# Kernel optimization log

Hardware: AMD Instinct MI355X
Metric: run time of the kernel (lower is better)

## Reference

```python
import jax, jax.numpy as jnp
import numpy as np

NUM_SYMBOLS = 100000
EMBED_DIM = 256
DIM = 2 * EMBED_DIM          # 512
NUM_HEADS = 4
HEAD_DIM = DIM // NUM_HEADS  # 128
N = 100                      # hard-coded neighbor count in source
EPS = 1e-5


def layernorm(x, g, b):
    mu = jnp.mean(x, axis=-1, keepdims=True)
    var = jnp.var(x, axis=-1, keepdims=True)
    return (x - mu) * jax.lax.rsqrt(var + EPS) * g + b


def setup_inputs() -> dict:
    key = jax.random.key(0)
    ks = jax.random.split(key, 12)
    B, FEW = 512, 2
    connections = jax.random.randint(ks[0], (B, FEW, N, 2), 0, NUM_SYMBOLS)
    mask = jax.random.randint(ks[1], (B * FEW, N, N), 0, 2).astype(jnp.int32)
    s = 0.02
    emb = jax.random.normal(ks[2], (NUM_SYMBOLS + 1, EMBED_DIM), jnp.float32) * s
    qkv_w = jax.random.normal(ks[3], (3 * DIM, DIM), jnp.float32) * s
    qkv_b = jnp.zeros((3 * DIM,), jnp.float32)
    proj_w = jax.random.normal(ks[4], (DIM, DIM), jnp.float32) * s
    proj_b = jnp.zeros((DIM,), jnp.float32)
    ln1_g = jnp.ones((DIM,), jnp.float32); ln1_b = jnp.zeros((DIM,), jnp.float32)
    ln2_g = jnp.ones((DIM,), jnp.float32); ln2_b = jnp.zeros((DIM,), jnp.float32)
    fc_w = jax.random.normal(ks[5], (DIM // 2, DIM), jnp.float32) * s
    fc_b = jnp.zeros((DIM // 2,), jnp.float32)
    return {"connections": connections, "mask": mask, "emb": emb,
            "qkv_w": qkv_w, "qkv_b": qkv_b, "proj_w": proj_w, "proj_b": proj_b,
            "ln1_g": ln1_g, "ln1_b": ln1_b, "ln2_g": ln2_g, "ln2_b": ln2_b,
            "fc_w": fc_w, "fc_b": fc_b}


def reference(connections, mask, emb, qkv_w, qkv_b, proj_w, proj_b,
              ln1_g, ln1_b, ln2_g, ln2_b, fc_w, fc_b):
    # embedding gathers for (relation, entity) pairs
    rel = emb[connections[..., 0]]          # [B, few, N, E]
    ent = emb[connections[..., 1]]          # [B, few, N, E]
    x = jnp.concatenate([rel, ent], axis=-1).reshape(-1, N, DIM)  # [BN, N, C]
    m = mask.reshape(-1, N, N)

    xn = layernorm(x, ln1_g, ln1_b)
    qkv = xn @ qkv_w.T + qkv_b              # [BN, N, 3C]
    BN = xn.shape[0]
    qkv = qkv.reshape(BN, N, 3, NUM_HEADS, HEAD_DIM).transpose(2, 0, 3, 1, 4)
    q, k, v = qkv[0], qkv[1], qkv[2]        # [BN, H, N, hd]

    scale = HEAD_DIM ** -0.5
    attn = jnp.einsum('bhnd,bhmd->bhnm', q, k) * scale
    attn = jnp.where(m[:, None] == 0, -1e9, attn)
    attn = jax.nn.softmax(attn, axis=-1)    # [BN, H, N, N]

    y = jnp.einsum('bhnm,bhmd->bhnd', attn, v)
    y = y.transpose(0, 2, 1, 3).reshape(BN, N, DIM)
    y = y @ proj_w.T + proj_b               # [BN, N, C]

    # attn.mean(dim=2): mean over query axis -> [BN, H, N]; bmm with y
    wc = jnp.einsum('bhn,bnc->bhc', attn.mean(axis=2), y)   # [BN, H, C]
    out = layernorm(wc, ln2_g, ln2_b) @ fc_w.T + fc_b       # [BN, H, C//2]
    return out
```

## Files before the change

kernel.cpp:

```cpp
#include <hip/hip_runtime.h>
#include <stdint.h>

typedef __attribute__((ext_vector_type(8))) short bf16x8;
typedef __attribute__((ext_vector_type(4))) float f32x4;
typedef __attribute__((ext_vector_type(4))) unsigned int u32x4;
typedef __attribute__((ext_vector_type(4))) unsigned short u16x4;

typedef const void __attribute__((address_space(1))) gvoid_t;
typedef void __attribute__((address_space(3))) lvoid_t;

__device__ __forceinline__ unsigned short f2bf(float f) {
  union { float f; unsigned int u; } v; v.f = f;
  unsigned int u = v.u;
  u += 0x7fffu + ((u >> 16) & 1u);
  return (unsigned short)(u >> 16);
}
__device__ __forceinline__ float bf2f(unsigned short h) {
  union { unsigned int u; float f; } v; v.u = ((unsigned int)h) << 16;
  return v.f;
}
__device__ __forceinline__ void load_lds16(const void* g, void* l) {
  __builtin_amdgcn_global_load_lds((gvoid_t*)g, (lvoid_t*)l, 16, 0, 0);
}

#define GATE6() asm volatile("s_waitcnt vmcnt(6)" ::: "memory")
#define GATE4() asm volatile("s_waitcnt vmcnt(4)" ::: "memory")
#define GATE0() asm volatile("s_waitcnt vmcnt(0)" ::: "memory")
#define BARRIER()                    \
  do {                               \
    asm volatile("" ::: "memory");   \
    __builtin_amdgcn_s_barrier();    \
    asm volatile("" ::: "memory");   \
  } while (0)

__global__ __launch_bounds__(256) void k_cvt(const float* __restrict__ src,
                                             unsigned short* __restrict__ dst, int n) {
  int i = blockIdx.x * 256 + threadIdx.x;
  if (i < n) dst[i] = f2bf(src[i]);
}

__global__ __launch_bounds__(256) void k_maskpack(const int* __restrict__ mask,
                                                  unsigned int* __restrict__ bm) {
  const int lane = threadIdx.x & 63;
  const int wv = (blockIdx.x << 2) + (threadIdx.x >> 6);
  const int r0 = wv * 16;
  for (int i = 0; i < 16; ++i) {
    const int r = r0 + i;
    const size_t base = (size_t)r * 100;
    const int c0 = mask[base + lane];
    int c1 = 0;
    if (lane < 36) c1 = mask[base + 64 + lane];
    const unsigned long long b0 = __ballot(c0 != 0);
    const unsigned long long b1 = __ballot(c1 != 0);
    if (lane == 0) {
      u32x4 v;
      v[0] = (unsigned int)b0; v[1] = (unsigned int)(b0 >> 32);
      v[2] = (unsigned int)b1; v[3] = (unsigned int)(b1 >> 32);
      *(u32x4*)(bm + (size_t)r * 4) = v;
    }
  }
}

__global__ __launch_bounds__(256) void k_gather_ln(const int* __restrict__ conn,
                                                   const float* __restrict__ emb,
                                                   const float* __restrict__ g1,
                                                   const float* __restrict__ b1,
                                                   unsigned short* __restrict__ xn,
                                                   int row0) {
  const int lane = threadIdx.x & 63;
  const int wid = threadIdx.x >> 6;
  const int rloc = blockIdx.x * 4 + wid;
  const int row = row0 + rloc;
  const int rel = conn[row * 2 + 0];
  const int ent = conn[row * 2 + 1];
  const float4 r4 = *(const float4*)(emb + (size_t)rel * 256 + lane * 4);
  const float4 e4 = *(const float4*)(emb + (size_t)ent * 256 + lane * 4);
  float rv[4] = {r4.x, r4.y, r4.z, r4.w};
  float ev[4] = {e4.x, e4.y, e4.z, e4.w};
  float s = 0.f, ss = 0.f;
#pragma unroll
  for (int j = 0; j < 4; ++j) { s += rv[j] + ev[j]; ss += rv[j] * rv[j] + ev[j] * ev[j]; }
#pragma unroll
  for (int d = 1; d < 64; d <<= 1) { s += __shfl_xor(s, d, 64); ss += __shfl_xor(ss, d, 64); }
  const float mu = s * (1.f / 512.f);
  const float var = ss * (1.f / 512.f) - mu * mu;
  const float rs = rsqrtf(var + 1e-5f);
  const float4 ga = *(const float4*)(g1 + lane * 4);
  const float4 gb = *(const float4*)(g1 + 256 + lane * 4);
  const float4 ba = *(const float4*)(b1 + lane * 4);
  const float4 bb = *(const float4*)(b1 + 256 + lane * 4);
  float gav[4] = {ga.x, ga.y, ga.z, ga.w}, gbv[4] = {gb.x, gb.y, gb.z, gb.w};
  float bav[4] = {ba.x, ba.y, ba.z, ba.w}, bbv[4] = {bb.x, bb.y, bb.z, bb.w};
  u16x4 o0, o1;
#pragma unroll
  for (int j = 0; j < 4; ++j) {
    o0[j] = f2bf((rv[j] - mu) * rs * gav[j] + bav[j]);
    o1[j] = f2bf((ev[j] - mu) * rs * gbv[j] + bbv[j]);
  }
  unsigned short* orow = xn + (size_t)rloc * 512;
  *(u16x4*)(orow + lane * 4) = o0;
  *(u16x4*)(orow + 256 + lane * 4) = o1;
}

__global__ __launch_bounds__(256, 2) void k_gemm4(const unsigned short* __restrict__ A,
                                                  const unsigned short* __restrict__ W,
                                                  const float* __restrict__ bias,
                                                  unsigned short* __restrict__ C,
                                                  int N, int K, int ntiles, int nwg) {
  __shared__ __align__(16) unsigned short ldsA[3][256 * 32];
  __shared__ __align__(16) unsigned short ldsB[3][128 * 32];

  const int orig = blockIdx.x;
  const int q = nwg >> 3, r = nwg & 7;
  const int xcd = orig & 7, idx = orig >> 3;
  const int wg = (xcd < r ? xcd * (q + 1) : r * (q + 1) + (xcd - r) * q) + idx;
  const int mtile = wg / ntiles, ntile = wg % ntiles;

  const int t = threadIdx.x, lane = t & 63, wid = t >> 6;
  const int wm = wid >> 1, wn = wid & 1;
  const size_t Abase = (size_t)mtile * 256 * K;
  const size_t Wbase = (size_t)ntile * 128 * K;
  const int NT = K >> 5;

  f32x4 acc[8][4];
#pragma unroll
  for (int i = 0; i < 8; ++i)
#pragma unroll
    for (int j = 0; j < 4; ++j) acc[i][j] = (f32x4){0.f, 0.f, 0.f, 0.f};

  const int sr0 = t >> 2;
  auto stage = [&](int buf, int kt) {
#pragma unroll
    for (int it = 0; it < 4; ++it) {
      const int row = it * 64 + sr0;
      const int cl = (t & 3) ^ ((row >> 1) & 3);
      load_lds16(A + Abase + (size_t)row * K + kt * 32 + cl * 8, &ldsA[buf][it * 2048 + t * 8]);
    }
#pragma unroll
    for (int it = 0; it < 2; ++it) {
      const int row = it * 64 + sr0;
      const int cl = (t & 3) ^ ((row >> 1) & 3);
      load_lds16(W + Wbase + (size_t)row * K + kt * 32 + cl * 8, &ldsB[buf][it * 2048 + t * 8]);
    }
  };

  stage(0, 0);
  stage(1, 1);

  int cur = 0;
  for (int kt = 0; kt < NT; ++kt) {
    if (kt + 1 < NT) { GATE6(); } else { GATE0(); }
    BARRIER();
    if (kt + 2 < NT) {
      int s2 = cur + 2; if (s2 >= 3) s2 -= 3;
      stage(s2, kt + 2);
    }
    bf16x8 af[8], bfr[4];
#pragma unroll
    for (int mi = 0; mi < 8; ++mi) {
      const int row = wm * 128 + mi * 16 + (lane & 15);
      const int st = (lane >> 4) ^ ((row >> 1) & 3);
      af[mi] = *(const bf16x8*)&ldsA[cur][row * 32 + st * 8];
    }
#pragma unroll
    for (int ni = 0; ni < 4; ++ni) {
      const int row = wn * 64 + ni * 16 + (lane & 15);
      const int st = (lane >> 4) ^ ((row >> 1) & 3);
      bfr[ni] = *(const bf16x8*)&ldsB[cur][row * 32 + st * 8];
    }
#pragma unroll
    for (int mi = 0; mi < 8; ++mi)
#pragma unroll
      for (int ni = 0; ni < 4; ++ni)
        acc[mi][ni] = __builtin_amdgcn_mfma_f32_16x16x32_bf16(bfr[ni], af[mi], acc[mi][ni], 0, 0, 0);
    cur = (cur + 1 == 3) ? 0 : cur + 1;
  }

#pragma unroll
  for (int ni = 0; ni < 4; ++ni) {
    const int colb = ntile * 128 + wn * 64 + ni * 16 + ((lane >> 4) << 2);
    const float4 bv = *(const float4*)(bias + colb);
#pragma unroll
    for (int mi = 0; mi < 8; ++mi) {
      const int row = mtile * 256 + wm * 128 + mi * 16 + (lane & 15);
      const unsigned int lo =
          (unsigned int)f2bf(acc[mi][ni][0] + bv.x) | ((unsigned int)f2bf(acc[mi][ni][1] + bv.y) << 16);
      const unsigned int hi =
          (unsigned int)f2bf(acc[mi][ni][2] + bv.z) | ((unsigned int)f2bf(acc[mi][ni][3] + bv.w) << 16);
      uint2 pk; pk.x = lo; pk.y = hi;
      *(uint2*)(C + (size_t)row * N + colb) = pk;
    }
  }
}

template <typename CT>
__global__ __launch_bounds__(256) void k_gemm3(const unsigned short* __restrict__ A,
                                               const unsigned short* __restrict__ W,
                                               const float* __restrict__ bias,
                                               CT* __restrict__ C,
                                               int N, int K, int ntiles, int nwg) {
  __shared__ __align__(16) unsigned short ldsA[3][128 * 32];
  __shared__ __align__(16) unsigned short ldsB[3][128 * 32];

  const int orig = blockIdx.x;
  const int q = nwg >> 3, r = nwg & 7;
  const int xcd = orig & 7, idx = orig >> 3;
  const int wg = (xcd < r ? xcd * (q + 1) : r * (q + 1) + (xcd - r) * q) + idx;
  const int mtile = wg / ntiles, ntile = wg % ntiles;

  const int t = threadIdx.x, lane = t & 63, wid = t >> 6;
  const int wm = wid >> 1, wn = wid & 1;
  const size_t Abase = (size_t)mtile * 128 * K;
  const size_t Wbase = (size_t)ntile * 128 * K;
  const int NT = K >> 5;

  f32x4 acc[4][4];
#pragma unroll
  for (int i = 0; i < 4; ++i)
#pragma unroll
    for (int j = 0; j < 4; ++j) acc[i][j] = (f32x4){0.f, 0.f, 0.f, 0.f};

  const int sr0 = t >> 2;
  auto stage = [&](int buf, int kt) {
#pragma unroll
    for (int it = 0; it < 2; ++it) {
      const int row = it * 64 + sr0;
      const int cl = (t & 3) ^ ((row >> 1) & 3);
      load_lds16(A + Abase + (size_t)row * K + kt * 32 + cl * 8, &ldsA[buf][it * 2048 + t * 8]);
    }
#pragma unroll
    for (int it = 0; it < 2; ++it) {
      const int row = it * 64 + sr0;
      const int cl = (t & 3) ^ ((row >> 1) & 3);
      load_lds16(W + Wbase + (size_t)row * K + kt * 32 + cl * 8, &ldsB[buf][it * 2048 + t * 8]);
    }
  };

  stage(0, 0);
  stage(1, 1);

  int cur = 0;
  for (int kt = 0; kt < NT; ++kt) {
    if (kt + 1 < NT) { GATE4(); } else { GATE0(); }
    BARRIER();
    if (kt + 2 < NT) {
      int s2 = cur + 2; if (s2 >= 3) s2 -= 3;
      stage(s2, kt + 2);
    }
    bf16x8 af[4], bfr[4];
#pragma unroll
    for (int mi = 0; mi < 4; ++mi) {
      const int row = wm * 64 + mi * 16 + (lane & 15);
      const int st = (lane >> 4) ^ ((row >> 1) & 3);
      af[mi] = *(const bf16x8*)&ldsA[cur][row * 32 + st * 8];
    }
#pragma unroll
    for (int ni = 0; ni < 4; ++ni) {
      const int row = wn * 64 + ni * 16 + (lane & 15);
      const int st = (lane >> 4) ^ ((row >> 1) & 3);
      bfr[ni] = *(const bf16x8*)&ldsB[cur][row * 32 + st * 8];
    }
#pragma unroll
    for (int mi = 0; mi < 4; ++mi)
#pragma unroll
      for (int ni = 0; ni < 4; ++ni)
        acc[mi][ni] = __builtin_amdgcn_mfma_f32_16x16x32_bf16(af[mi], bfr[ni], acc[mi][ni], 0, 0, 0);
    cur = (cur + 1 == 3) ? 0 : cur + 1;
  }

#pragma unroll
  for (int ni = 0; ni < 4; ++ni) {
    const int col = ntile * 128 + wn * 64 + ni * 16 + (lane & 15);
    const float bv = bias[col];
#pragma unroll
    for (int mi = 0; mi < 4; ++mi) {
      const int row0 = mtile * 128 + wm * 64 + mi * 16 + ((lane >> 4) << 2);
#pragma unroll
      for (int r2 = 0; r2 < 4; ++r2) {
        const float ov = acc[mi][ni][r2] + bv;
        if constexpr (sizeof(CT) == 2)
          C[(size_t)(row0 + r2) * N + col] = (CT)f2bf(ov);
        else
          C[(size_t)(row0 + r2) * N + col] = (CT)ov;
      }
    }
  }
}

__global__ __launch_bounds__(512) void k_attn(const unsigned short* __restrict__ qkv,
                                              const unsigned int* __restrict__ bm,
                                              unsigned short* __restrict__ y,
                                              float* __restrict__ am, int b0) {
  __shared__ __align__(16) unsigned short A_lds[128 * 128];
  __shared__ __align__(16) unsigned short P_lds[7 * 16 * 128];
  __shared__ float am_s[112];
  const int t = threadIdx.x, lane = t & 63, w = t >> 6;
  const int bl = blockIdx.x >> 2, h = blockIdx.x & 3;
  const int bg = b0 + bl;
  const unsigned short* qk = qkv + (size_t)bl * 153600;

  if (t < 112) am_s[t] = 0.f;

#pragma unroll
  for (int j = 0; j < 4; ++j) {
    const int row = j * 32 + w * 4 + (lane >> 4);
    if (row < 100) {
      const int c = (lane & 15) ^ (row & 7);
      load_lds16(qk + (size_t)row * 1536 + 512 + h * 128 + c * 8,
                 &A_lds[j * 4096 + w * 512 + lane * 8]);
    }
  }
  u32x4 vv[4];
#pragma unroll
  for (int p = 0; p < 4; ++p) {
    const int vm = p * 32 + (t >> 4);
    const u32x4 z = {0u, 0u, 0u, 0u};
    vv[p] = (vm < 100) ? *(const u32x4*)(qk + (size_t)vm * 1536 + 1024 + h * 128 + (t & 15) * 8) : z;
  }
  bf16x8 qf[4];
  {
    const int qrow = w * 16 + (lane & 15);
    const bool qv = (w < 7) && (qrow < 100);
#pragma unroll
    for (int kk = 0; kk < 4; ++kk) {
      const bf16x8 z = {0, 0, 0, 0, 0, 0, 0, 0};
      qf[kk] = qv ? *(const bf16x8*)(qk + (size_t)qrow * 1536 + h * 128 + kk * 32 + (lane >> 4) * 8) : z;
    }
  }
  if (t < 192) {
    const u32x4 z = {0u, 0u, 0u, 0u};
    *(u32x4*)&A_lds[(100 + (t >> 4)) * 128 + (t & 15) * 8] = z;
  }
  __syncthreads();

  f32x4 sa[7];
#pragma unroll
  for (int ni = 0; ni < 7; ++ni) sa[ni] = (f32x4){0.f, 0.f, 0.f, 0.f};
  if (w < 7) {
#pragma unroll
    for (int kk = 0; kk < 4; ++kk)
#pragma unroll
      for (int ni = 0; ni < 7; ++ni) {
        const int row = ni * 16 + (lane & 15);
        const int c = (kk * 4 + (lane >> 4)) ^ (row & 7);
        const bf16x8 kf = *(const bf16x8*)&A_lds[row * 128 + (c << 3)];
        sa[ni] = __builtin_amdgcn_mfma_f32_16x16x32_bf16(qf[kk], kf, sa[ni], 0, 0, 0);
      }
  }
  __syncthreads();

#pragma unroll
  for (int p = 0; p < 4; ++p) {
    const int vm = p * 32 + (t >> 4);
    unsigned short tmp[8];
    *(u32x4*)tmp = vv[p];
#pragma unroll
    for (int jj = 0; jj < 8; ++jj) {
      const int d = (lane & 15) * 8 + jj;
      const int swz = (vm >> 3) ^ (((d >> 3) ^ d) & 7);
      A_lds[d * 128 + swz * 8 + (vm & 7)] = tmp[jj];
    }
  }

  if (w < 7) {
    const float scale = 0.08838834764831843f;
    float psum[7] = {0.f, 0.f, 0.f, 0.f, 0.f, 0.f, 0.f};
#pragma unroll
    for (int r = 0; r < 4; ++r) {
      const int lr = (lane >> 4) * 4 + r;
      const int qrow = w * 16 + lr;
      if (qrow < 100) {
        const u32x4 bmv = *(const u32x4*)(bm + ((size_t)bg * 100 + qrow) * 4);
        float x[7];
#pragma unroll
        for (int ni = 0; ni < 7; ++ni) {
          const int col = ni * 16 + (lane & 15);
          const unsigned int bit = (bmv[ni >> 1] >> (((ni & 1) << 4) + (lane & 15))) & 1u;
          x[ni] = (col < 100) ? (bit ? sa[ni][r] * scale : -1e9f) : -1e30f;
        }
        float mx = x[0];
#pragma unroll
        for (int ni = 1; ni < 7; ++ni) mx = fmaxf(mx, x[ni]);
#pragma unroll
        for (int dd = 1; dd < 16; dd <<= 1) mx = fmaxf(mx, __shfl_xor(mx, dd, 64));
        float e[7], sum = 0.f;
#pragma unroll
        for (int ni = 0; ni < 7; ++ni) { e[ni] = __expf(x[ni] - mx); sum += e[ni]; }
#pragma unroll
        for (int dd = 1; dd < 16; dd <<= 1) sum += __shfl_xor(sum, dd, 64);
        const float inv = 1.f / sum;
#pragma unroll
        for (int ni = 0; ni < 7; ++ni) {
          const float pv = e[ni] * inv;
          psum[ni] += pv;
          const int col = ni * 16 + (lane & 15);
          const int c = (col >> 3) ^ (lr & 7);
          P_lds[w * 2048 + lr * 128 + c * 8 + (col & 7)] = f2bf(pv);
        }
      } else {
#pragma unroll
        for (int ni = 0; ni < 7; ++ni) {
          const int col = ni * 16 + (lane & 15);
          const int c = (col >> 3) ^ (lr & 7);
          P_lds[w * 2048 + lr * 128 + c * 8 + (col & 7)] = 0;
        }
      }
    }
    if (lane < 32) {
      const int lr = lane & 15;
      const int c = (14 + (lane >> 4)) ^ (lr & 7);
      const u32x4 z = {0u, 0u, 0u, 0u};
      *(u32x4*)&P_lds[w * 2048 + lr * 128 + c * 8] = z;
    }
#pragma unroll
    for (int ni = 0; ni < 7; ++ni) atomicAdd(&am_s[ni * 16 + (lane & 15)], psum[ni]);
  }
  __syncthreads();

  if (t < 100) am[((size_t)bg * 4 + h) * 100 + t] = am_s[t] * 0.01f;

  if (w < 7) {
#pragma unroll
    for (int dt = 0; dt < 8; ++dt) {
      f32x4 acc = {0.f, 0.f, 0.f, 0.f};
#pragma unroll
      for (int kk = 0; kk < 4; ++kk) {
        const int c = kk * 4 + (lane >> 4);
        const bf16x8 pf = *(const bf16x8*)&P_lds[w * 2048 + (lane & 15) * 128 + ((c ^ (lane & 7)) << 3)];
        const int d = dt * 16 + (lane & 15);
        const int cv = c ^ (((d >> 3) ^ d) & 7);
        const bf16x8 vf = *(const bf16x8*)&A_lds[d * 128 + (cv << 3)];
        acc = __builtin_amdgcn_mfma_f32_16x16x32_bf16(pf, vf, acc, 0, 0, 0);
      }
      const int d = dt * 16 + (lane & 15);
#pragma unroll
      for (int r = 0; r < 4; ++r) {
        const int qrow = w * 16 + (lane >> 4) * 4 + r;
        if (qrow < 100)
          y[((size_t)bl * 100 + qrow) * 512 + h * 128 + d] = f2bf(acc[r]);
      }
    }
  }
}

__global__ __launch_bounds__(256) void k_z(const float* __restrict__ am,
                                           const unsigned short* __restrict__ y,
                                           unsigned short* __restrict__ zb, int b0) {
  __shared__ float ams[400];
  const int bl = blockIdx.x, t = threadIdx.x;
  const int bg = b0 + bl;
  for (int i = t; i < 400; i += 256) ams[i] = am[(size_t)bg * 400 + i];
  __syncthreads();
  float a0[4] = {0, 0, 0, 0}, a1[4] = {0, 0, 0, 0};
  const unsigned short* yb = y + (size_t)bl * 100 * 512 + t * 2;
  for (int n = 0; n < 100; ++n) {
    const unsigned int u = *(const unsigned int*)(yb + (size_t)n * 512);
    const float v0 = bf2f((unsigned short)(u & 0xffffu));
    const float v1 = bf2f((unsigned short)(u >> 16));
#pragma unroll
    for (int hh = 0; hh < 4; ++hh) {
      const float ww = ams[hh * 100 + n];
      a0[hh] += ww * v0;
      a1[hh] += ww * v1;
    }
  }
#pragma unroll
  for (int hh = 0; hh < 4; ++hh) {
    const unsigned int pk = (unsigned int)f2bf(a0[hh]) | ((unsigned int)f2bf(a1[hh]) << 16);
    *(unsigned int*)(zb + ((size_t)(bl * 4 + hh)) * 512 + 2 * t) = pk;
  }
}

__global__ __launch_bounds__(256) void k_ln2(const unsigned short* __restrict__ wcb,
                                             const float* __restrict__ g2,
                                             const float* __restrict__ b2,
                                             unsigned short* __restrict__ wcn) {
  const int t = threadIdx.x, lane = t & 63, w = t >> 6;
  const int row = blockIdx.x * 4 + w;
  const u32x4 pv = *(const u32x4*)(wcb + (size_t)row * 512 + lane * 8);
  float v[8];
#pragma unroll
  for (int j = 0; j < 4; ++j) {
    v[2 * j] = bf2f((unsigned short)(pv[j] & 0xffffu));
    v[2 * j + 1] = bf2f((unsigned short)(pv[j] >> 16));
  }
  float s = 0.f, ss = 0.f;
#pragma unroll
  for (int j = 0; j < 8; ++j) { s += v[j]; ss += v[j] * v[j]; }
#pragma unroll
  for (int d = 1; d < 64; d <<= 1) { s += __shfl_xor(s, d, 64); ss += __shfl_xor(ss, d, 64); }
  const float mu = s * (1.f / 512.f);
  const float var = ss * (1.f / 512.f) - mu * mu;
  const float rs = rsqrtf(var + 1e-5f);
  const float4 ga = *(const float4*)(g2 + lane * 8);
  const float4 gb = *(const float4*)(g2 + lane * 8 + 4);
  const float4 ba = *(const float4*)(b2 + lane * 8);
  const float4 bb = *(const float4*)(b2 + lane * 8 + 4);
  const float gv[8] = {ga.x, ga.y, ga.z, ga.w, gb.x, gb.y, gb.z, gb.w};
  const float bv[8] = {ba.x, ba.y, ba.z, ba.w, bb.x, bb.y, bb.z, bb.w};
  u32x4 ov;
#pragma unroll
  for (int j = 0; j < 4; ++j) {
    const unsigned short lo = f2bf((v[2 * j] - mu) * rs * gv[2 * j] + bv[2 * j]);
    const unsigned short hi = f2bf((v[2 * j + 1] - mu) * rs * gv[2 * j + 1] + bv[2 * j + 1]);
    ov[j] = (unsigned int)lo | ((unsigned int)hi << 16);
  }
  *(u32x4*)(wcn + (size_t)row * 512 + lane * 8) = ov;
}

extern "C" void kernel_launch(void* const* d_in, const int* in_sizes, int n_in,
                              void* d_out, int out_size, void* d_ws, size_t ws_size,
                              hipStream_t stream) {
  const int* conn = (const int*)d_in[0];
  const int* mask = (const int*)d_in[1];
  const float* emb = (const float*)d_in[2];
  const float* qkv_w = (const float*)d_in[3];
  const float* qkv_b = (const float*)d_in[4];
  const float* proj_w = (const float*)d_in[5];
  const float* proj_b = (const float*)d_in[6];
  const float* ln1g = (const float*)d_in[7];
  const float* ln1b = (const float*)d_in[8];
  const float* ln2g = (const float*)d_in[9];
  const float* ln2b = (const float*)d_in[10];
  const float* fc_w = (const float*)d_in[11];
  const float* fc_b = (const float*)d_in[12];
  float* out = (float*)d_out;

  size_t off = 0;
  auto alloc = [&](size_t bytes) {
    void* p = (char*)d_ws + off;
    off += (bytes + 255) & ~(size_t)255;
    return p;
  };
  unsigned short* w_qkv = (unsigned short*)alloc((size_t)1536 * 512 * 2);
  unsigned short* w_proj = (unsigned short*)alloc((size_t)512 * 512 * 2);
  unsigned short* w_fc = (unsigned short*)alloc((size_t)256 * 512 * 2);
  float* am = (float*)alloc((size_t)1024 * 400 * 4);
  unsigned int* bmb = (unsigned int*)alloc((size_t)102400 * 16);
  const size_t fixed = off;

  int CB = 512;
  while (CB > 64) {
    size_t need = fixed + (size_t)CB * 4 * 512 * 2 * 3 + (size_t)CB * 100 * 512 * 2 +
                  (size_t)CB * 100 * 1536 * 2 + 4096;
    if (need <= ws_size) break;
    CB >>= 1;
  }
  unsigned short* zbuf = (unsigned short*)alloc((size_t)CB * 4 * 512 * 2);
  unsigned short* wcb = (unsigned short*)alloc((size_t)CB * 4 * 512 * 2);
  unsigned short* wcn = (unsigned short*)alloc((size_t)CB * 4 * 512 * 2);
  unsigned short* xn = (unsigned short*)alloc((size_t)CB * 100 * 512 * 2);
  unsigned short* qkvb = (unsigned short*)alloc((size_t)CB * 100 * 1536 * 2);

  k_cvt<<<(786432 + 255) / 256, 256, 0, stream>>>(qkv_w, w_qkv, 786432);
  k_cvt<<<(262144 + 255) / 256, 256, 0, stream>>>(proj_w, w_proj, 262144);
  k_cvt<<<(131072 + 255) / 256, 256, 0, stream>>>(fc_w, w_fc, 131072);
  k_maskpack<<<1600, 256, 0, stream>>>(mask, bmb);

  for (int b0 = 0; b0 < 1024; b0 += CB) {
    const int mt256 = CB * 100 / 256;
    const int zt = CB * 4 / 128;
    k_gather_ln<<<CB * 25, 256, 0, stream>>>(conn, emb, ln1g, ln1b, xn, b0 * 100);
    k_gemm4<<<12 * mt256, 256, 0, stream>>>(xn, w_qkv, qkv_b, qkvb, 1536, 512, 12, 12 * mt256);
    k_attn<<<CB * 4, 512, 0, stream>>>(qkvb, bmb, xn , am, b0);
    k_z<<<CB, 256, 0, stream>>>(am, xn , zbuf, b0);
    k_gemm3<unsigned short><<<4 * zt, 256, 0, stream>>>(zbuf, w_proj, proj_b, wcb, 512, 512, 4, 4 * zt);
    k_ln2<<<CB, 256, 0, stream>>>(wcb, ln2g, ln2b, wcn);
    k_gemm3<float><<<2 * zt, 256, 0, stream>>>(wcn, w_fc, fc_b, out + (size_t)b0 * 1024, 256, 512, 2, 2 * zt);
  }
}
```

Before: 577.1 us.

## Warp-specialize QKV GEMM with producer waves and LDS flag sync

Replaces the QKV GEMM's barrier-synchronized triple-buffered loop with a warp-specialized design: two extra producer waves stream A/W tiles into a 4-slot LDS ring while four consumer waves run MFMAs, coordinating through LDS ready/done counters with spin-sleep. It also merges the three weight conversion launches into one and raises the chunk size so the batch can run in a single pass if workspace allows. The aim is to overlap global loads with compute and cut block barriers and launch overhead. The cost is higher LDS use (occupancy), spin-wait overhead, and reliance on correct vmcnt ordering for the flags.

Result: slower. 628.9 us (+9.0%).

```diff
diff --git a/kernel.cpp b/kernel.cpp
--- a/kernel.cpp
+++ b/kernel.cpp
@@ -23,9 +23,11 @@
   __builtin_amdgcn_global_load_lds((gvoid_t*)g, (lvoid_t*)l, 16, 0, 0);
 }
 
-#define GATE6() asm volatile("s_waitcnt vmcnt(6)" ::: "memory")
+#define GATE12() asm volatile("s_waitcnt vmcnt(12)" ::: "memory")
 #define GATE4() asm volatile("s_waitcnt vmcnt(4)" ::: "memory")
 #define GATE0() asm volatile("s_waitcnt vmcnt(0)" ::: "memory")
+#define LGKM0() asm volatile("s_waitcnt lgkmcnt(0)" ::: "memory")
+#define CFENCE() asm volatile("" ::: "memory")
 #define BARRIER()                    \
   do {                               \
     asm volatile("" ::: "memory");   \
@@ -33,10 +35,18 @@
     asm volatile("" ::: "memory");   \
   } while (0)
 
-__global__ __launch_bounds__(256) void k_cvt(const float* __restrict__ src,
-                                             unsigned short* __restrict__ dst, int n) {
+__global__ __launch_bounds__(256) void k_cvt3(const float* __restrict__ s0, int n0,
+                                              const float* __restrict__ s1, int n1,
+                                              const float* __restrict__ s2, int n2,
+                                              unsigned short* __restrict__ d0,
+                                              unsigned short* __restrict__ d1,
+                                              unsigned short* __restrict__ d2) {
   int i = blockIdx.x * 256 + threadIdx.x;
-  if (i < n) dst[i] = f2bf(src[i]);
+  if (i < n0) { d0[i] = f2bf(s0[i]); return; }
+  i -= n0;
+  if (i < n1) { d1[i] = f2bf(s1[i]); return; }
+  i -= n1;
+  if (i < n2) d2[i] = f2bf(s2[i]);
 }
 
 __global__ __launch_bounds__(256) void k_maskpack(const int* __restrict__ mask,
@@ -102,13 +112,15 @@
   *(u16x4*)(orow + 256 + lane * 4) = o1;
 }
 
-__global__ __launch_bounds__(256, 2) void k_gemm4(const unsigned short* __restrict__ A,
-                                                  const unsigned short* __restrict__ W,
-                                                  const float* __restrict__ bias,
-                                                  unsigned short* __restrict__ C,
-                                                  int N, int K, int ntiles, int nwg) {
-  __shared__ __align__(16) unsigned short ldsA[3][256 * 32];
-  __shared__ __align__(16) unsigned short ldsB[3][128 * 32];
+__global__ __launch_bounds__(384) void k_gemm5(const unsigned short* __restrict__ A,
+                                               const unsigned short* __restrict__ W,
+                                               const float* __restrict__ bias,
+                                               unsigned short* __restrict__ C,
+                                               int N, int K, int ntiles, int nwg) {
+  __shared__ __align__(16) unsigned short slotA[4][256 * 32];
+  __shared__ __align__(16) unsigned short slotB[4][128 * 32];
+  __shared__ int rdy[32];
+  __shared__ int done[32];
 
   const int orig = blockIdx.x;
   const int q = nwg >> 3, r = nwg & 7;
@@ -117,63 +129,80 @@
   const int mtile = wg / ntiles, ntile = wg % ntiles;
 
   const int t = threadIdx.x, lane = t & 63, wid = t >> 6;
-  const int wm = wid >> 1, wn = wid & 1;
   const size_t Abase = (size_t)mtile * 256 * K;
   const size_t Wbase = (size_t)ntile * 128 * K;
   const int NT = K >> 5;
 
+  if (t < 32) { rdy[t] = 0; done[t] = 0; }
+  BARRIER();
+
+  if (wid >= 4) {
+    const int pt = t - 256;
+    for (int s = 0; s < NT; ++s) {
+      if (s >= 4) {
+        volatile int* dv = done;
+        while (dv[s - 4] < 4) __builtin_amdgcn_s_sleep(1);
+        CFENCE();
+      }
+      const int slot = s & 3;
+#pragma unroll
+      for (int it = 0; it < 8; ++it) {
+        const int row = it * 32 + (pt >> 2);
+        const int cl = (pt & 3) ^ ((row >> 1) & 3);
+        load_lds16(A + Abase + (size_t)row * K + s * 32 + cl * 8, &slotA[slot][it * 1024 + pt * 8]);
+      }
+#pragma unroll
+      for (int it = 0; it < 4; ++it) {
+        const int row = it * 32 + (pt >> 2);
+        const int cl = (pt & 3) ^ ((row >> 1) & 3);
+        load_lds16(W + Wbase + (size_t)row * K + s * 32 + cl * 8, &slotB[slot][it * 1024 + pt * 8]);
+      }
+      if (s >= 1) {
+        GATE12();
+        atomicAdd(&rdy[s - 1], 1);
+        CFENCE();
+      }
+    }
+    GATE0();
+    atomicAdd(&rdy[NT - 1], 1);
+    return;
+  }
+
+  const int wm = wid >> 1, wn = wid & 1;
   f32x4 acc[8][4];
 #pragma unroll
   for (int i = 0; i < 8; ++i)
 #pragma unroll
     for (int j = 0; j < 4; ++j) acc[i][j] = (f32x4){0.f, 0.f, 0.f, 0.f};
 
-  const int sr0 = t >> 2;
-  auto stage = [&](int buf, int kt) {
-#pragma unroll
-    for (int it = 0; it < 4; ++it) {
-      const int row = it * 64 + sr0;
-      const int cl = (t & 3) ^ ((row >> 1) & 3);
-      load_lds16(A + Abase + (size_t)row * K + kt * 32 + cl * 8, &ldsA[buf][it * 2048 + t * 8]);
-    }
-#pragma unroll
-    for (int it = 0; it < 2; ++it) {
-      const int row = it * 64 + sr0;
-      const int cl = (t & 3) ^ ((row >> 1) & 3);
-      load_lds16(W + Wbase + (size_t)row * K + kt * 32 + cl * 8, &ldsB[buf][it * 2048 + t * 8]);
-    }
-  };
-
-  stage(0, 0);
-  stage(1, 1);
-
-  int cur = 0;
-  for (int kt = 0; kt < NT; ++kt) {
-    if (kt + 1 < NT) { GATE6(); } else { GATE0(); }
-    BARRIER();
-    if (kt + 2 < NT) {
-      int s2 = cur + 2; if (s2 >= 3) s2 -= 3;
-      stage(s2, kt + 2);
-    }
-    bf16x8 af[8], bfr[4];
+  for (int s = 0; s < NT; ++s) {
+    {
+      volatile int* rv = rdy;
+      while (rv[s] < 2) __builtin_amdgcn_s_sleep(1);
+      CFENCE();
+    }
+    const int slot = s & 3;
+    bf16x8 af[8], br[4];
 #pragma unroll
     for (int mi = 0; mi < 8; ++mi) {
       const int row = wm * 128 + mi * 16 + (lane & 15);
       const int st = (lane >> 4) ^ ((row >> 1) & 3);
-      af[mi] = *(const bf16x8*)&ldsA[cur][row * 32 + st * 8];
+      af[mi] = *(const bf16x8*)&slotA[slot][row * 32 + st * 8];
     }
 #pragma unroll
     for (int ni = 0; ni < 4; ++ni) {
       const int row = wn * 64 + ni * 16 + (lane & 15);
       const int st = (lane >> 4) ^ ((row >> 1) & 3);
-      bfr[ni] = *(const bf16x8*)&ldsB[cur][row * 32 + st * 8];
+      br[ni] = *(const bf16x8*)&slotB[slot][row * 32 + st * 8];
     }
 #pragma unroll
     for (int mi = 0; mi < 8; ++mi)
 #pragma unroll
       for (int ni = 0; ni < 4; ++ni)
-        acc[mi][ni] = __builtin_amdgcn_mfma_f32_16x16x32_bf16(bfr[ni], af[mi], acc[mi][ni], 0, 0, 0);
-    cur = (cur + 1 == 3) ? 0 : cur + 1;
+        acc[mi][ni] = __builtin_amdgcn_mfma_f32_16x16x32_bf16(br[ni], af[mi], acc[mi][ni], 0, 0, 0);
+    LGKM0();
+    atomicAdd(&done[s], 1);
+    CFENCE();
   }
 
 #pragma unroll
@@ -539,10 +568,10 @@
   unsigned int* bmb = (unsigned int*)alloc((size_t)102400 * 16);
   const size_t fixed = off;
 
-  int CB = 512;
+  int CB = 1024;
   while (CB > 64) {
     size_t need = fixed + (size_t)CB * 4 * 512 * 2 * 3 + (size_t)CB * 100 * 512 * 2 +
-                  (size_t)CB * 100 * 1536 * 2 + 4096;
+                  (size_t)CB * 100 * 1536 * 2 + 8192;
     if (need <= ws_size) break;
     CB >>= 1;
   }
@@ -552,16 +581,15 @@
   unsigned short* xn = (unsigned short*)alloc((size_t)CB * 100 * 512 * 2);
   unsigned short* qkvb = (unsigned short*)alloc((size_t)CB * 100 * 1536 * 2);
 
-  k_cvt<<<(786432 + 255) / 256, 256, 0, stream>>>(qkv_w, w_qkv, 786432);
-  k_cvt<<<(262144 + 255) / 256, 256, 0, stream>>>(proj_w, w_proj, 262144);
-  k_cvt<<<(131072 + 255) / 256, 256, 0, stream>>>(fc_w, w_fc, 131072);
+  k_cvt3<<<(786432 + 262144 + 131072 + 255) / 256, 256, 0, stream>>>(
+      qkv_w, 786432, proj_w, 262144, fc_w, 131072, w_qkv, w_proj, w_fc);
   k_maskpack<<<1600, 256, 0, stream>>>(mask, bmb);
 
   for (int b0 = 0; b0 < 1024; b0 += CB) {
     const int mt256 = CB * 100 / 256;
     const int zt = CB * 4 / 128;
     k_gather_ln<<<CB * 25, 256, 0, stream>>>(conn, emb, ln1g, ln1b, xn, b0 * 100);
-    k_gemm4<<<12 * mt256, 256, 0, stream>>>(xn, w_qkv, qkv_b, qkvb, 1536, 512, 12, 12 * mt256);
+    k_gemm5<<<12 * mt256, 384, 0, stream>>>(xn, w_qkv, qkv_b, qkvb, 1536, 512, 12, 12 * mt256);
     k_attn<<<CB * 4, 512, 0, stream>>>(qkvb, bmb, xn , am, b0);
     k_z<<<CB, 256, 0, stream>>>(am, xn , zbuf, b0);
     k_gemm3<unsigned short><<<4 * zt, 256, 0, stream>>>(zbuf, w_proj, proj_b, wcb, 512, 512, 4, 4 * zt);
```
